# Optimization experiments

Measured on AMD Instinct MI355X. Metric: run time of the kernel, lower is better.

The kernel has to match this reference:

```python
import jax, jax.numpy as jnp
import numpy as np

NUM_CATEGORIES = 64
INPUT_DIM = 256
HIDDEN_DIM = 256
N = 4096  # number of samples (each with its own category)
M = 16    # rows per sample


def setup_inputs() -> dict:
    key = jax.random.key(0)
    k_x, k_cat, k_W = jax.random.split(key, 3)
    x = jax.random.normal(k_x, (N, M, INPUT_DIM), dtype=jnp.float32)
    cat_ids = jax.random.randint(k_cat, (N,), 0, NUM_CATEGORIES, dtype=jnp.int64)
    W = 0.02 * jax.random.normal(k_W, (NUM_CATEGORIES, INPUT_DIM, HIDDEN_DIM), dtype=jnp.float32)
    b = jnp.zeros((NUM_CATEGORIES, HIDDEN_DIM), dtype=jnp.float32)
    return {"x": x, "cat_ids": cat_ids, "W": W, "b": b}


def reference(x, cat_ids, W, b):
    # Gather per-sample weights/biases, then batched matmul + bias add.
    selected_W = W[cat_ids]              # [N, input_dim, hidden_dim]
    selected_b = b[cat_ids]              # [N, hidden_dim]
    out = jnp.einsum('nmi,nih->nmh', x, selected_W) + selected_b[:, None, :]
    return out
```

## Files before the change

### kernel.cpp

```cpp
#include <hip/hip_runtime.h>
#include <hip/hip_bf16.h>
#include <stdint.h>

#define N_SAMPLES 4096
#define M_ROWS 16
#define K_DIM 256
#define H_DIM 256
#define N_CATS 64
#define SPB 4
#define MAX_PADDED (N_SAMPLES + N_CATS * (SPB - 1))
#define NGROUP (MAX_PADDED / SPB)
#define GPX (NGROUP / 8)

typedef _Float16 half8 __attribute__((ext_vector_type(8)));
typedef _Float16 half4 __attribute__((ext_vector_type(4)));
typedef float floatx4 __attribute__((ext_vector_type(4)));

#define GLOAD_LDS(g, l)                                          \
  __builtin_amdgcn_global_load_lds(                              \
      (const __attribute__((address_space(1))) void*)(g),        \
      (__attribute__((address_space(3))) void*)(l), 16, 0, 0)

#define WT_BYTES ((size_t)N_CATS * K_DIM * H_DIM * 2)
#define GCAT_OFF WT_BYTES
#define ORD_OFF  (WT_BYTES + 4288)
#define WS_NEED  (ORD_OFF + (size_t)MAX_PADDED * 4)

__global__ __launch_bounds__(256)
void prep_combined(const float* __restrict__ W, _Float16* __restrict__ Wt,
                   const int* __restrict__ cat, int* __restrict__ ord,
                   int* __restrict__ gcat) {
  const int tid = threadIdx.x;
  if (blockIdx.x < 1024) {
    __shared__ _Float16 t[64][72];
    const int bid = blockIdx.x;
    const int c  = bid >> 4;
    const int kb = (bid >> 2) & 3;
    const int hb = bid & 3;
    const int r  = tid >> 2;
    const int cg = (tid & 3) * 16;
    const float* src = W + ((size_t)c << 16) + (size_t)(kb * 64 + r) * 256 + hb * 64 + cg;
#pragma unroll
    for (int j = 0; j < 16; j += 4) {
      float4 v = *(const float4*)(src + j);
      t[r][cg + j + 0] = (_Float16)v.x;
      t[r][cg + j + 1] = (_Float16)v.y;
      t[r][cg + j + 2] = (_Float16)v.z;
      t[r][cg + j + 3] = (_Float16)v.w;
    }
    __syncthreads();
    _Float16* dst = Wt + ((size_t)c << 16) + (size_t)(hb * 64 + r) * 256 + kb * 64 + cg;
    half8 o0, o1;
#pragma unroll
    for (int j = 0; j < 8; j++) o0[j] = t[cg + j][r];
#pragma unroll
    for (int j = 0; j < 8; j++) o1[j] = t[cg + 8 + j][r];
    *(half8*)(dst) = o0;
    *(half8*)(dst + 8) = o1;
  } else {
    __shared__ int hist[N_CATS];
    __shared__ int poffs[N_CATS];
    __shared__ int curs[N_CATS];
    if (tid < N_CATS) hist[tid] = 0;
    for (int i = tid; i < MAX_PADDED; i += 256) ord[i] = -1;
    for (int i = tid; i < NGROUP; i += 256) gcat[i] = 0;
    __syncthreads();
    for (int i = tid; i < N_SAMPLES; i += 256) atomicAdd(&hist[cat[i]], 1);
    __syncthreads();
    if (tid == 0) {
      int run = 0;
      for (int c = 0; c < N_CATS; c++) {
        poffs[c] = run;
        run += ((hist[c] + SPB - 1) / SPB) * SPB;
      }
    }
    if (tid < N_CATS) curs[tid] = 0;
    __syncthreads();
    if (tid < N_CATS) {
      const int c = tid;
      const int g0 = poffs[c] >> 2;
      const int ng = (hist[c] + SPB - 1) >> 2;
      for (int g = 0; g < ng; g++) gcat[g0 + g] = c;
    }
    for (int i = tid; i < N_SAMPLES; i += 256) {
      int c = cat[i];
      int p = poffs[c] + atomicAdd(&curs[c], 1);
      ord[p] = i;
    }
  }
}

__global__ __launch_bounds__(512, 4)
void gemm_kernel(const float* __restrict__ x, const float* __restrict__ bias,
                 const _Float16* __restrict__ Wt, const int* __restrict__ ord,
                 const int* __restrict__ gcat, float* __restrict__ out) {
  __shared__ __align__(16) float sA[64 * 256];

  const int tid = threadIdx.x;
  const int B = blockIdx.x;
  const int xcd = B & 7;
  const int group = xcd * GPX + (B >> 3);

  const int cat = gcat[group];
  const int4 sm = *(const int4*)(ord + group * 4);
  if (sm.x < 0) return;

  const int wid  = tid >> 6;
  const int lane = tid & 63;
  const int l15  = lane & 15;
  const int quad = lane >> 4;

  const int s0 = sm.x;
  const int s1 = sm.y < 0 ? sm.x : sm.y;
  const int s2 = sm.z < 0 ? sm.x : sm.z;
  const int s3 = sm.w < 0 ? sm.x : sm.w;
  const int lx = (lane ^ wid) << 2;
#pragma unroll
  for (int i = 0; i < 8; i++) {
    const int smp = ((i >> 1) == 0) ? s0 : ((i >> 1) == 1) ? s1 : ((i >> 1) == 2) ? s2 : s3;
    const float* gp = x + ((size_t)smp << 12) + (size_t)((i & 1) * 8 + wid) * 256 + lx;
    GLOAD_LDS(gp, sA + (i * 8 + wid) * 256);
  }

  const _Float16* wb = Wt + ((size_t)cat << 16) + (size_t)(wid * 32 + l15) * K_DIM + quad * 8;
  half8 bf[8][2];
#pragma unroll
  for (int kt = 0; kt < 4; kt++) {
    bf[kt][0] = *(const half8*)(wb + kt * 32);
    bf[kt][1] = *(const half8*)(wb + 16 * K_DIM + kt * 32);
  }
  const float bv0 = bias[cat * H_DIM + wid * 32 + l15];
  const float bv1 = bias[cat * H_DIM + wid * 32 + 16 + l15];

  floatx4 acc[4][2];
#pragma unroll
  for (int i = 0; i < 4; i++)
#pragma unroll
    for (int j = 0; j < 2; j++)
#pragma unroll
      for (int e = 0; e < 4; e++) acc[i][j][e] = 0.0f;

  __syncthreads();

  const int swz = (l15 & 7) << 2;
#pragma unroll
  for (int kt = 0; kt < 8; kt++) {
    if (kt < 4) {
      bf[kt + 4][0] = *(const half8*)(wb + (kt + 4) * 32);
      bf[kt + 4][1] = *(const half8*)(wb + 16 * K_DIM + (kt + 4) * 32);
    }
    half8 af[4];
#pragma unroll
    for (int mt = 0; mt < 4; mt++) {
      const float* ap = sA + (size_t)(mt * 16 + l15) * 256;
      float4 f0 = *(const float4*)(ap + ((kt * 32 + quad * 8 + 0) ^ swz));
      float4 f1 = *(const float4*)(ap + ((kt * 32 + quad * 8 + 4) ^ swz));
      af[mt][0] = (_Float16)f0.x; af[mt][1] = (_Float16)f0.y;
      af[mt][2] = (_Float16)f0.z; af[mt][3] = (_Float16)f0.w;
      af[mt][4] = (_Float16)f1.x; af[mt][5] = (_Float16)f1.y;
      af[mt][6] = (_Float16)f1.z; af[mt][7] = (_Float16)f1.w;
    }
#pragma unroll
    for (int mt = 0; mt < 4; mt++) {
      acc[mt][0] = __builtin_amdgcn_mfma_f32_16x16x32_f16(af[mt], bf[kt][0], acc[mt][0], 0, 0, 0);
      acc[mt][1] = __builtin_amdgcn_mfma_f32_16x16x32_f16(af[mt], bf[kt][1], acc[mt][1], 0, 0, 0);
    }
  }

  const int srow[4] = {sm.x, sm.y, sm.z, sm.w};
#pragma unroll
  for (int mt = 0; mt < 4; mt++) {
    const int s = srow[mt];
    if (s < 0) continue;
    float* obase = out + ((size_t)s << 12);
#pragma unroll
    for (int nt = 0; nt < 2; nt++) {
      const int col = wid * 32 + nt * 16 + l15;
      const float bv = nt ? bv1 : bv0;
#pragma unroll
      for (int rr = 0; rr < 4; rr++) {
        const int row = quad * 4 + rr;
        __builtin_nontemporal_store(acc[mt][nt][rr] + bv, obase + (size_t)row * H_DIM + col);
      }
    }
  }
}

__global__ __launch_bounds__(256)
void naive_kernel(const float* __restrict__ x, const int* __restrict__ cat,
                  const float* __restrict__ W, const float* __restrict__ bias,
                  float* __restrict__ out) {
  __shared__ float sx[16 * 256];
  const int n = blockIdx.x;
  const int tid = threadIdx.x;
  const int c = cat[n];
  const float* xs = x + (size_t)n * 16 * 256;
  for (int i = tid; i < 16 * 256; i += 256) sx[i] = xs[i];
  __syncthreads();
  const float* Wc = W + ((size_t)c << 16);
  float accv[16];
  float bv = bias[c * 256 + tid];
#pragma unroll
  for (int m = 0; m < 16; m++) accv[m] = bv;
  for (int k = 0; k < 256; k++) {
    float w = Wc[(size_t)k * 256 + tid];
#pragma unroll
    for (int m = 0; m < 16; m++) accv[m] += sx[m * 256 + k] * w;
  }
#pragma unroll
  for (int m = 0; m < 16; m++) out[((size_t)n * 16 + m) * 256 + tid] = accv[m];
}

extern "C" void kernel_launch(void* const* d_in, const int* in_sizes, int n_in,
                              void* d_out, int out_size, void* d_ws, size_t ws_size,
                              hipStream_t stream) {
  const float* x    = (const float*)d_in[0];
  const int*   cat  = (const int*)d_in[1];
  const float* W    = (const float*)d_in[2];
  const float* bias = (const float*)d_in[3];
  float* out = (float*)d_out;

  if (ws_size < WS_NEED) {
    naive_kernel<<<N_SAMPLES, 256, 0, stream>>>(x, cat, W, bias, out);
    return;
  }

  char* ws = (char*)d_ws;
  _Float16* Wt = (_Float16*)ws;
  int* gcat = (int*)(ws + GCAT_OFF);
  int* ord  = (int*)(ws + ORD_OFF);

  prep_combined<<<1025, 256, 0, stream>>>(W, Wt, cat, ord, gcat);
  gemm_kernel<<<NGROUP, 512, 0, stream>>>(x, bias, Wt, ord, gcat, out);
}
```

Measured before the change: 168.2 us.

## Stage activations as fp16 in padded LDS via register loads instead of async fp32 copy

Replaces the direct global-to-LDS fp32 copy of activations with register loads that convert x to fp16 once and store it into a padded LDS tile (row stride 264 halves), so the inner loop reads half8 directly with no per-tile conversion or swizzle. This halves the LDS footprint, and the launch bound is raised to 8 blocks per CU to use the freed space for occupancy. A sched_barrier keeps the weight loads ahead of the activation loads, and the nontemporal output stores become plain stores. The trade-off is that the x load now goes through registers and is no longer asynchronous, and the higher occupancy target may force register spills.

```diff
diff --git a/kernel.cpp b/kernel.cpp
--- a/kernel.cpp
+++ b/kernel.cpp
@@ -11,15 +11,11 @@
 #define MAX_PADDED (N_SAMPLES + N_CATS * (SPB - 1))
 #define NGROUP (MAX_PADDED / SPB)
 #define GPX (NGROUP / 8)
+#define AROW 264
 
 typedef _Float16 half8 __attribute__((ext_vector_type(8)));
 typedef _Float16 half4 __attribute__((ext_vector_type(4)));
 typedef float floatx4 __attribute__((ext_vector_type(4)));
-
-#define GLOAD_LDS(g, l)                                          \
-  __builtin_amdgcn_global_load_lds(                              \
-      (const __attribute__((address_space(1))) void*)(g),        \
-      (__attribute__((address_space(3))) void*)(l), 16, 0, 0)
 
 #define WT_BYTES ((size_t)N_CATS * K_DIM * H_DIM * 2)
 #define GCAT_OFF WT_BYTES
@@ -90,11 +86,11 @@
   }
 }
 
-__global__ __launch_bounds__(512, 4)
+__global__ __launch_bounds__(512, 8)
 void gemm_kernel(const float* __restrict__ x, const float* __restrict__ bias,
                  const _Float16* __restrict__ Wt, const int* __restrict__ ord,
                  const int* __restrict__ gcat, float* __restrict__ out) {
-  __shared__ __align__(16) float sA[64 * 256];
+  __shared__ __align__(16) _Float16 sA[64 * AROW];
 
   const int tid = threadIdx.x;
   const int B = blockIdx.x;
@@ -110,18 +106,6 @@
   const int l15  = lane & 15;
   const int quad = lane >> 4;
 
-  const int s0 = sm.x;
-  const int s1 = sm.y < 0 ? sm.x : sm.y;
-  const int s2 = sm.z < 0 ? sm.x : sm.z;
-  const int s3 = sm.w < 0 ? sm.x : sm.w;
-  const int lx = (lane ^ wid) << 2;
-#pragma unroll
-  for (int i = 0; i < 8; i++) {
-    const int smp = ((i >> 1) == 0) ? s0 : ((i >> 1) == 1) ? s1 : ((i >> 1) == 2) ? s2 : s3;
-    const float* gp = x + ((size_t)smp << 12) + (size_t)((i & 1) * 8 + wid) * 256 + lx;
-    GLOAD_LDS(gp, sA + (i * 8 + wid) * 256);
-  }
-
   const _Float16* wb = Wt + ((size_t)cat << 16) + (size_t)(wid * 32 + l15) * K_DIM + quad * 8;
   half8 bf[8][2];
 #pragma unroll
@@ -131,6 +115,30 @@
   }
   const float bv0 = bias[cat * H_DIM + wid * 32 + l15];
   const float bv1 = bias[cat * H_DIM + wid * 32 + 16 + l15];
+  __builtin_amdgcn_sched_barrier(0);
+
+  const int smp = (wid >> 1 == 0) ? sm.x : (wid >> 1 == 1) ? sm.y : (wid >> 1 == 2) ? sm.z : sm.w;
+  const float* asrc = (smp >= 0)
+      ? (x + ((size_t)smp << 12) + (size_t)((wid & 1) * 8) * 256)
+      : nullptr;
+  _Float16* adst = sA + (size_t)(wid * 8) * AROW;
+  if (asrc) {
+#pragma unroll
+    for (int j = 0; j < 8; j++) {
+      float4 v = *(const float4*)(asrc + j * 256 + lane * 4);
+      half4 h;
+      h[0] = (_Float16)v.x; h[1] = (_Float16)v.y;
+      h[2] = (_Float16)v.z; h[3] = (_Float16)v.w;
+      *(half4*)(adst + (size_t)j * AROW + lane * 4) = h;
+    }
+  } else {
+    half4 h;
+#pragma unroll
+    for (int e = 0; e < 4; e++) h[e] = (_Float16)0.0f;
+#pragma unroll
+    for (int j = 0; j < 8; j++)
+      *(half4*)(adst + (size_t)j * AROW + lane * 4) = h;
+  }
 
   floatx4 acc[4][2];
 #pragma unroll
@@ -142,7 +150,6 @@
 
   __syncthreads();
 
-  const int swz = (l15 & 7) << 2;
 #pragma unroll
   for (int kt = 0; kt < 8; kt++) {
     if (kt < 4) {
@@ -151,15 +158,8 @@
     }
     half8 af[4];
 #pragma unroll
-    for (int mt = 0; mt < 4; mt++) {
-      const float* ap = sA + (size_t)(mt * 16 + l15) * 256;
-      float4 f0 = *(const float4*)(ap + ((kt * 32 + quad * 8 + 0) ^ swz));
-      float4 f1 = *(const float4*)(ap + ((kt * 32 + quad * 8 + 4) ^ swz));
-      af[mt][0] = (_Float16)f0.x; af[mt][1] = (_Float16)f0.y;
-      af[mt][2] = (_Float16)f0.z; af[mt][3] = (_Float16)f0.w;
-      af[mt][4] = (_Float16)f1.x; af[mt][5] = (_Float16)f1.y;
-      af[mt][6] = (_Float16)f1.z; af[mt][7] = (_Float16)f1.w;
-    }
+    for (int mt = 0; mt < 4; mt++)
+      af[mt] = *(const half8*)&sA[(size_t)(mt * 16 + l15) * AROW + kt * 32 + quad * 8];
 #pragma unroll
     for (int mt = 0; mt < 4; mt++) {
       acc[mt][0] = __builtin_amdgcn_mfma_f32_16x16x32_f16(af[mt], bf[kt][0], acc[mt][0], 0, 0, 0);
@@ -180,7 +180,7 @@
 #pragma unroll
       for (int rr = 0; rr < 4; rr++) {
         const int row = quad * 4 + rr;
-        __builtin_nontemporal_store(acc[mt][nt][rr] + bv, obase + (size_t)row * H_DIM + col);
+        obase[(size_t)row * H_DIM + col] = acc[mt][nt][rr] + bv;
       }
     }
   }
```

New measurement: 181.6 us. 1.08x slower.

## Halve gemm block to 4 waves, each computing two column halves sequentially

Applied to the files above, without the earlier changes.

The GEMM kernel drops from 512 threads (8 waves) to 256 threads (4 waves) per block. Each wave now loads one sample's x tile into LDS and sweeps the output columns in two passes of 128, writing the first half mid-loop before resetting the accumulators. A 5-slot rotating register buffer prefetches the weight fragments across both passes. The swizzle and bias handling are adjusted to match, and output stores become plain stores instead of nontemporal ones. This trades per-block thread parallelism for more work per wave and fewer blocks' worth of waves, aiming to reduce register and launch overhead and improve latency hiding.

```diff
diff --git a/kernel.cpp b/kernel.cpp
--- a/kernel.cpp
+++ b/kernel.cpp
@@ -90,10 +90,10 @@
   }
 }
 
-__global__ __launch_bounds__(512, 4)
-void gemm_kernel(const float* __restrict__ x, const float* __restrict__ bias,
-                 const _Float16* __restrict__ Wt, const int* __restrict__ ord,
-                 const int* __restrict__ gcat, float* __restrict__ out) {
+__global__ __launch_bounds__(256, 2)
+void gemm_f32(const float* __restrict__ x, const float* __restrict__ bias,
+              const _Float16* __restrict__ Wt, const int* __restrict__ ord,
+              const int* __restrict__ gcat, float* __restrict__ out) {
   __shared__ __align__(16) float sA[64 * 256];
 
   const int tid = threadIdx.x;
@@ -110,27 +110,31 @@
   const int l15  = lane & 15;
   const int quad = lane >> 4;
 
-  const int s0 = sm.x;
-  const int s1 = sm.y < 0 ? sm.x : sm.y;
-  const int s2 = sm.z < 0 ? sm.x : sm.z;
-  const int s3 = sm.w < 0 ? sm.x : sm.w;
-  const int lx = (lane ^ wid) << 2;
-#pragma unroll
-  for (int i = 0; i < 8; i++) {
-    const int smp = ((i >> 1) == 0) ? s0 : ((i >> 1) == 1) ? s1 : ((i >> 1) == 2) ? s2 : s3;
-    const float* gp = x + ((size_t)smp << 12) + (size_t)((i & 1) * 8 + wid) * 256 + lx;
-    GLOAD_LDS(gp, sA + (i * 8 + wid) * 256);
-  }
-
-  const _Float16* wb = Wt + ((size_t)cat << 16) + (size_t)(wid * 32 + l15) * K_DIM + quad * 8;
-  half8 bf[8][2];
+  const _Float16* wb0 = Wt + ((size_t)cat << 16) +
+                        (size_t)(wid * 32 + l15) * K_DIM + quad * 8;
+  const _Float16* wb1 = wb0 + (size_t)128 * K_DIM;
+
+  half8 bf[5][2];
 #pragma unroll
   for (int kt = 0; kt < 4; kt++) {
-    bf[kt][0] = *(const half8*)(wb + kt * 32);
-    bf[kt][1] = *(const half8*)(wb + 16 * K_DIM + kt * 32);
-  }
-  const float bv0 = bias[cat * H_DIM + wid * 32 + l15];
-  const float bv1 = bias[cat * H_DIM + wid * 32 + 16 + l15];
+    bf[kt][0] = *(const half8*)(wb0 + kt * 32);
+    bf[kt][1] = *(const half8*)(wb0 + 16 * K_DIM + kt * 32);
+  }
+  float bv[2][2];
+#pragma unroll
+  for (int p = 0; p < 2; p++)
+#pragma unroll
+    for (int nt = 0; nt < 2; nt++)
+      bv[p][nt] = bias[cat * H_DIM + p * 128 + wid * 32 + nt * 16 + l15];
+  __builtin_amdgcn_sched_barrier(0);
+
+  const int smp0 = (wid == 0) ? sm.x : (wid == 1) ? sm.y : (wid == 2) ? sm.z : sm.w;
+  const int smp  = (smp0 >= 0) ? smp0 : sm.x;
+  const float* xs = x + ((size_t)smp << 12);
+  float* adst = sA + wid * (16 * 256);
+#pragma unroll
+  for (int j = 0; j < 16; j++)
+    GLOAD_LDS(xs + j * 256 + ((lane ^ (j & 7)) << 2), adst + j * 256);
 
   floatx4 acc[4][2];
 #pragma unroll
@@ -142,19 +146,27 @@
 
   __syncthreads();
 
-  const int swz = (l15 & 7) << 2;
-#pragma unroll
-  for (int kt = 0; kt < 8; kt++) {
-    if (kt < 4) {
-      bf[kt + 4][0] = *(const half8*)(wb + (kt + 4) * 32);
-      bf[kt + 4][1] = *(const half8*)(wb + 16 * K_DIM + (kt + 4) * 32);
-    }
+  const int srow[4] = {sm.x, sm.y, sm.z, sm.w};
+  const int v = l15 & 7;
+
+#pragma unroll
+  for (int g = 0; g < 16; g++) {
+    if (g < 12) {
+      const int gn = g + 4;
+      const _Float16* wbn = (gn < 8) ? wb0 : wb1;
+      const int ktn = gn & 7;
+      bf[gn % 5][0] = *(const half8*)(wbn + ktn * 32);
+      bf[gn % 5][1] = *(const half8*)(wbn + 16 * K_DIM + ktn * 32);
+      __builtin_amdgcn_sched_barrier(0);
+    }
+    const int kt = g & 7;
     half8 af[4];
 #pragma unroll
     for (int mt = 0; mt < 4; mt++) {
       const float* ap = sA + (size_t)(mt * 16 + l15) * 256;
-      float4 f0 = *(const float4*)(ap + ((kt * 32 + quad * 8 + 0) ^ swz));
-      float4 f1 = *(const float4*)(ap + ((kt * 32 + quad * 8 + 4) ^ swz));
+      const int s0 = kt * 8 + quad * 2;
+      float4 f0 = *(const float4*)(ap + ((s0 ^ v) << 2));
+      float4 f1 = *(const float4*)(ap + (((s0 + 1) ^ v) << 2));
       af[mt][0] = (_Float16)f0.x; af[mt][1] = (_Float16)f0.y;
       af[mt][2] = (_Float16)f0.z; af[mt][3] = (_Float16)f0.w;
       af[mt][4] = (_Float16)f1.x; af[mt][5] = (_Float16)f1.y;
@@ -162,12 +174,33 @@
     }
 #pragma unroll
     for (int mt = 0; mt < 4; mt++) {
-      acc[mt][0] = __builtin_amdgcn_mfma_f32_16x16x32_f16(af[mt], bf[kt][0], acc[mt][0], 0, 0, 0);
-      acc[mt][1] = __builtin_amdgcn_mfma_f32_16x16x32_f16(af[mt], bf[kt][1], acc[mt][1], 0, 0, 0);
-    }
-  }
-
-  const int srow[4] = {sm.x, sm.y, sm.z, sm.w};
+      acc[mt][0] = __builtin_amdgcn_mfma_f32_16x16x32_f16(af[mt], bf[g % 5][0], acc[mt][0], 0, 0, 0);
+      acc[mt][1] = __builtin_amdgcn_mfma_f32_16x16x32_f16(af[mt], bf[g % 5][1], acc[mt][1], 0, 0, 0);
+    }
+
+    if (g == 7) {
+#pragma unroll
+      for (int mt = 0; mt < 4; mt++) {
+        const int s = srow[mt];
+        if (s < 0) continue;
+        float* obase = out + ((size_t)s << 12);
+#pragma unroll
+        for (int nt = 0; nt < 2; nt++) {
+          const int col = wid * 32 + nt * 16 + l15;
+#pragma unroll
+          for (int rr = 0; rr < 4; rr++)
+            obase[(size_t)(quad * 4 + rr) * H_DIM + col] = acc[mt][nt][rr] + bv[0][nt];
+        }
+      }
+#pragma unroll
+      for (int i = 0; i < 4; i++)
+#pragma unroll
+        for (int j = 0; j < 2; j++)
+#pragma unroll
+          for (int e = 0; e < 4; e++) acc[i][j][e] = 0.0f;
+    }
+  }
+
 #pragma unroll
   for (int mt = 0; mt < 4; mt++) {
     const int s = srow[mt];
@@ -175,13 +208,10 @@
     float* obase = out + ((size_t)s << 12);
 #pragma unroll
     for (int nt = 0; nt < 2; nt++) {
-      const int col = wid * 32 + nt * 16 + l15;
-      const float bv = nt ? bv1 : bv0;
-#pragma unroll
-      for (int rr = 0; rr < 4; rr++) {
-        const int row = quad * 4 + rr;
-        __builtin_nontemporal_store(acc[mt][nt][rr] + bv, obase + (size_t)row * H_DIM + col);
-      }
+      const int col = 128 + wid * 32 + nt * 16 + l15;
+#pragma unroll
+      for (int rr = 0; rr < 4; rr++)
+        obase[(size_t)(quad * 4 + rr) * H_DIM + col] = acc[mt][nt][rr] + bv[1][nt];
     }
   }
 }
@@ -231,5 +261,5 @@
   int* ord  = (int*)(ws + ORD_OFF);
 
   prep_combined<<<1025, 256, 0, stream>>>(W, Wt, cat, ord, gcat);
-  gemm_kernel<<<NGROUP, 512, 0, stream>>>(x, bias, Wt, ord, gcat, out);
-}
+  gemm_f32<<<NGROUP, 256, 0, stream>>>(x, bias, Wt, ord, gcat, out);
+}
```

Result: faster. 163.3 us (-2.9%).
